# Kernel optimization log

Measured on AMD Instinct MI355X. Metric: run time of the kernel, lower is better.

The kernel has to match this reference:

```python
import jax, jax.numpy as jnp
import numpy as np

ANCHOR_NUM = 8
CLASS_NUM = 2
IN_DIM = 1024

def setup_inputs() -> dict:
    key = jax.random.key(0)
    k1, k2, k3, k4 = jax.random.split(key, 4)
    batch_input = jax.random.normal(k1, (64, 512, IN_DIM), dtype=jnp.float32)
    # labels in {-1, 0, 1}: -1 = padding, 0 = negative anchor, 1 = positive anchor
    anchor_labels = jax.random.randint(k2, (64, 512, ANCHOR_NUM), 0, 3, dtype=jnp.int64 if jax.config.read('jax_enable_x64') else jnp.int32) - 1
    lim = 1.0 / np.sqrt(IN_DIM)
    W = jax.random.uniform(k3, (IN_DIM, ANCHOR_NUM * CLASS_NUM), dtype=jnp.float32, minval=-lim, maxval=lim)
    b = jax.random.uniform(k4, (ANCHOR_NUM * CLASS_NUM,), dtype=jnp.float32, minval=-lim, maxval=lim)
    return {"batch_input": batch_input, "W": W, "b": b, "anchor_labels": anchor_labels}

def reference(batch_input, W, b, anchor_labels):
    B, S, _ = batch_input.shape
    # logits: (B, S, anchor_num, class_num)
    logits = (jnp.einsum('bsd,dk->bsk', batch_input, W) + b).reshape(B, S, ANCHOR_NUM, CLASS_NUM)
    predict_label = jnp.argmax(logits, axis=3)  # (B, S, A)
    valid = (anchor_labels != -1)
    labels = jnp.maximum(anchor_labels, 0)  # safe class index for padded entries
    logp = jax.nn.log_softmax(logits, axis=-1)
    nll = -jnp.take_along_axis(logp, labels[..., None].astype(jnp.int32), axis=-1)[..., 0]
    # CrossEntropyLoss (mean) over all non-padding anchors == eval-path gather + CE
    vf = valid.astype(logits.dtype)
    loss = jnp.sum(nll * vf) / jnp.maximum(jnp.sum(vf), 1.0)
    # candidate mask stands in for candidate_idx (positive predictions, non-padding)
    candidate_mask = (predict_label == 1) & valid
    return loss, predict_label, candidate_mask
```

## Files before the change

kernel.cpp:

```cpp
#include <hip/hip_runtime.h>
#include <math.h>


#define ROWS   64
#define NW     8
#define KSLICE 128
#define CHUNK  32
#define NCH    (KSLICE/CHUNK)
#define XSTR   36
#define RSTR   136

__global__ __launch_bounds__(512, 4)
void rpn_main(const float* __restrict__ x, const float* __restrict__ W,
              const float* __restrict__ b, const int* __restrict__ lab,
              float* __restrict__ out, float* __restrict__ ws)
{
    __shared__ float xs[NW * ROWS * XSTR];
    float* red = xs;

    const int tid  = threadIdx.x;
    const int lane = tid & 63;
    const int ks   = __builtin_amdgcn_readfirstlane(tid >> 6);
    const int row0 = blockIdx.x * ROWS;

    float* slab = xs + ks * (ROWS * XSTR);
    const float* gbase = x + (size_t)row0 * 1024 + ks * KSLICE;

    float acc[16];
#pragma unroll
    for (int c = 0; c < 16; ++c) acc[c] = 0.f;

    float4 pf[8];
#pragma unroll
    for (int j = 0; j < 8; ++j) {
        int fl = j * 64 + lane;
        pf[j] = *(const float4*)(gbase + (size_t)(fl >> 3) * 1024 + (fl & 7) * 4);
    }

#pragma unroll 1
    for (int ch = 0; ch < NCH; ++ch) {
#pragma unroll
        for (int j = 0; j < 8; ++j) {
            int fl = j * 64 + lane;
            *(float4*)(slab + (fl >> 3) * XSTR + (fl & 7) * 4) = pf[j];
        }
        if (ch + 1 < NCH) {
            const float* g = gbase + (ch + 1) * CHUNK;
#pragma unroll
            for (int j = 0; j < 8; ++j) {
                int fl = j * 64 + lane;
                pf[j] = *(const float4*)(g + (size_t)(fl >> 3) * 1024 + (fl & 7) * 4);
            }
        }
        const float* xrow = slab + lane * XSTR;
        const float* wk   = W + (size_t)(ks * KSLICE + ch * CHUNK) * 16;
#pragma unroll
        for (int t4 = 0; t4 < 8; ++t4) {
            float4 xq = *(const float4*)(xrow + t4 * 4);
#pragma unroll
            for (int i = 0; i < 4; ++i) {
                float xv = (&xq.x)[i];
                const float* wr = wk + (t4 * 4 + i) * 16;
#pragma unroll
                for (int c = 0; c < 16; ++c)
                    acc[c] = fmaf(xv, wr[c], acc[c]);
            }
        }
    }

    __syncthreads();
    {
        float* rp = red + lane * RSTR + ks * 16;
        *(float4*)(rp + 0)  = make_float4(acc[0],  acc[1],  acc[2],  acc[3]);
        *(float4*)(rp + 4)  = make_float4(acc[4],  acc[5],  acc[6],  acc[7]);
        *(float4*)(rp + 8)  = make_float4(acc[8],  acc[9],  acc[10], acc[11]);
        *(float4*)(rp + 12) = make_float4(acc[12], acc[13], acc[14], acc[15]);
    }
    __syncthreads();

    if (tid < ROWS) {
        const int row = row0 + tid;
        float L[16];
#pragma unroll
        for (int c = 0; c < 16; ++c) {
            float s = 0.f;
#pragma unroll
            for (int k = 0; k < NW; ++k) s += red[tid * RSTR + k * 16 + c];
            L[c] = s + b[c];
        }

        const int* labp  = lab + (size_t)row * 8;
        float*     predp = out + 1 + (size_t)row * 8;
        float*     maskp = out + 1 + 262144 + (size_t)row * 8;

        float lsum = 0.f, lcnt = 0.f;
#pragma unroll
        for (int a = 0; a < 8; ++a) {
            float l0 = L[2 * a], l1 = L[2 * a + 1];
            int   lb = labp[a];
            int   pred  = (l1 > l0) ? 1 : 0;
            int   valid = (lb != -1);
            float m   = fmaxf(l0, l1);
            float lse = m + logf(expf(l0 - m) + expf(l1 - m));
            float nll = lse - ((lb == 1) ? l1 : l0);
            if (valid) { lsum += nll; lcnt += 1.f; }
            predp[a] = (float)pred;
            maskp[a] = (pred && valid) ? 1.f : 0.f;
        }

#pragma unroll
        for (int off = 32; off > 0; off >>= 1) {
            lsum += __shfl_down(lsum, off, 64);
            lcnt += __shfl_down(lcnt, off, 64);
        }
        if (tid == 0) {
            atomicAdd(&ws[0], lsum);
            atomicAdd(&ws[1], lcnt);
        }
    }
}

__global__ void rpn_final(const float* __restrict__ ws, float* __restrict__ out)
{
    out[0] = ws[0] / fmaxf(ws[1], 1.f);
}

extern "C" void kernel_launch(void* const* d_in, const int* in_sizes, int n_in,
                              void* d_out, int out_size, void* d_ws, size_t ws_size,
                              hipStream_t stream)
{
    const float* x   = (const float*)d_in[0];
    const float* W   = (const float*)d_in[1];
    const float* b   = (const float*)d_in[2];
    const int*   lab = (const int*)d_in[3];
    float* out = (float*)d_out;
    float* ws  = (float*)d_ws;

    hipMemsetAsync(ws, 0, 2 * sizeof(float), stream);
    rpn_main<<<dim3(512), dim3(512), 0, stream>>>(x, W, b, lab, out, ws);
    rpn_final<<<dim3(1), dim3(1), 0, stream>>>(ws, out);
}
```

Measured before the change: 237.9 us.

## Keep W slice in registers, stream rows directly, fuse final loss division

Drops the LDS-staged x tile. Each lane now holds a 4x16 slice of W in registers and streams one row at a time straight from global memory with a two-deep prefetch. Per-row results are reduced across lanes with a butterfly shuffle, and the logits pass uses one thread per anchor. The separate finalize kernel is replaced by a last-block-done atomic counter. In exchange there is heavy shuffle work per row and less row parallelism per block (32 rows, 4 waves).

```diff
diff --git a/kernel.cpp b/kernel.cpp
--- a/kernel.cpp
+++ b/kernel.cpp
@@ -2,127 +2,162 @@
 #include <math.h>
 
 
-#define ROWS   64
-#define NW     8
-#define KSLICE 128
-#define CHUNK  32
-#define NCH    (KSLICE/CHUNK)
-#define XSTR   36
-#define RSTR   136
+#define RPB 32
 
-__global__ __launch_bounds__(512, 4)
+__global__ __launch_bounds__(256, 2)
 void rpn_main(const float* __restrict__ x, const float* __restrict__ W,
               const float* __restrict__ b, const int* __restrict__ lab,
               float* __restrict__ out, float* __restrict__ ws)
 {
-    __shared__ float xs[NW * ROWS * XSTR];
-    float* red = xs;
+    __shared__ float red[4 * RPB * 16];
+    __shared__ float rsum[8];
 
     const int tid  = threadIdx.x;
     const int lane = tid & 63;
-    const int ks   = __builtin_amdgcn_readfirstlane(tid >> 6);
-    const int row0 = blockIdx.x * ROWS;
+    const int s    = __builtin_amdgcn_readfirstlane(tid >> 6);
+    const int row0 = blockIdx.x * RPB;
 
-    float* slab = xs + ks * (ROWS * XSTR);
-    const float* gbase = x + (size_t)row0 * 1024 + ks * KSLICE;
-
-    float acc[16];
+    float4 wc0[4], wc1[4], wc2[4], wc3[4];
+    {
+        const float* wp = W + (size_t)(s * 256 + lane * 4) * 16;
 #pragma unroll
-    for (int c = 0; c < 16; ++c) acc[c] = 0.f;
-
-    float4 pf[8];
-#pragma unroll
-    for (int j = 0; j < 8; ++j) {
-        int fl = j * 64 + lane;
-        pf[j] = *(const float4*)(gbase + (size_t)(fl >> 3) * 1024 + (fl & 7) * 4);
-    }
-
-#pragma unroll 1
-    for (int ch = 0; ch < NCH; ++ch) {
-#pragma unroll
-        for (int j = 0; j < 8; ++j) {
-            int fl = j * 64 + lane;
-            *(float4*)(slab + (fl >> 3) * XSTR + (fl & 7) * 4) = pf[j];
-        }
-        if (ch + 1 < NCH) {
-            const float* g = gbase + (ch + 1) * CHUNK;
-#pragma unroll
-            for (int j = 0; j < 8; ++j) {
-                int fl = j * 64 + lane;
-                pf[j] = *(const float4*)(g + (size_t)(fl >> 3) * 1024 + (fl & 7) * 4);
-            }
-        }
-        const float* xrow = slab + lane * XSTR;
-        const float* wk   = W + (size_t)(ks * KSLICE + ch * CHUNK) * 16;
-#pragma unroll
-        for (int t4 = 0; t4 < 8; ++t4) {
-            float4 xq = *(const float4*)(xrow + t4 * 4);
-#pragma unroll
-            for (int i = 0; i < 4; ++i) {
-                float xv = (&xq.x)[i];
-                const float* wr = wk + (t4 * 4 + i) * 16;
-#pragma unroll
-                for (int c = 0; c < 16; ++c)
-                    acc[c] = fmaf(xv, wr[c], acc[c]);
-            }
+        for (int q = 0; q < 4; ++q) {
+            wc0[q] = *(const float4*)(wp +  0 + q * 4);
+            wc1[q] = *(const float4*)(wp + 16 + q * 4);
+            wc2[q] = *(const float4*)(wp + 32 + q * 4);
+            wc3[q] = *(const float4*)(wp + 48 + q * 4);
         }
     }
 
-    __syncthreads();
-    {
-        float* rp = red + lane * RSTR + ks * 16;
-        *(float4*)(rp + 0)  = make_float4(acc[0],  acc[1],  acc[2],  acc[3]);
-        *(float4*)(rp + 4)  = make_float4(acc[4],  acc[5],  acc[6],  acc[7]);
-        *(float4*)(rp + 8)  = make_float4(acc[8],  acc[9],  acc[10], acc[11]);
-        *(float4*)(rp + 12) = make_float4(acc[12], acc[13], acc[14], acc[15]);
+    const float* xp = x + (size_t)row0 * 1024 + s * 256 + lane * 4;
+
+    float4 pfA = *(const float4*)(xp);
+    float4 pfB = *(const float4*)(xp + 1024);
+
+#pragma unroll 2
+    for (int r = 0; r < RPB; ++r) {
+        float4 xv = pfA;
+        pfA = pfB;
+        if (r + 2 < RPB) pfB = *(const float4*)(xp + (size_t)(r + 2) * 1024);
+
+        const float xs0 = xv.x, xs1 = xv.y, xs2 = xv.z, xs3 = xv.w;
+        float acc[16];
+#pragma unroll
+        for (int q = 0; q < 4; ++q) {
+            acc[4*q+0] = xs0 * wc0[q].x;
+            acc[4*q+1] = xs0 * wc0[q].y;
+            acc[4*q+2] = xs0 * wc0[q].z;
+            acc[4*q+3] = xs0 * wc0[q].w;
+        }
+#pragma unroll
+        for (int q = 0; q < 4; ++q) {
+            acc[4*q+0] = fmaf(xs1, wc1[q].x, acc[4*q+0]);
+            acc[4*q+1] = fmaf(xs1, wc1[q].y, acc[4*q+1]);
+            acc[4*q+2] = fmaf(xs1, wc1[q].z, acc[4*q+2]);
+            acc[4*q+3] = fmaf(xs1, wc1[q].w, acc[4*q+3]);
+        }
+#pragma unroll
+        for (int q = 0; q < 4; ++q) {
+            acc[4*q+0] = fmaf(xs2, wc2[q].x, acc[4*q+0]);
+            acc[4*q+1] = fmaf(xs2, wc2[q].y, acc[4*q+1]);
+            acc[4*q+2] = fmaf(xs2, wc2[q].z, acc[4*q+2]);
+            acc[4*q+3] = fmaf(xs2, wc2[q].w, acc[4*q+3]);
+        }
+#pragma unroll
+        for (int q = 0; q < 4; ++q) {
+            acc[4*q+0] = fmaf(xs3, wc3[q].x, acc[4*q+0]);
+            acc[4*q+1] = fmaf(xs3, wc3[q].y, acc[4*q+1]);
+            acc[4*q+2] = fmaf(xs3, wc3[q].z, acc[4*q+2]);
+            acc[4*q+3] = fmaf(xs3, wc3[q].w, acc[4*q+3]);
+        }
+
+        const bool h5 = (lane & 32) != 0;
+        float k8[8];
+#pragma unroll
+        for (int c = 0; c < 8; ++c) {
+            float keep = h5 ? acc[c + 8] : acc[c];
+            float send = h5 ? acc[c]     : acc[c + 8];
+            k8[c] = keep + __shfl_xor(send, 32, 64);
+        }
+        const bool h4 = (lane & 16) != 0;
+        float k4[4];
+#pragma unroll
+        for (int c = 0; c < 4; ++c) {
+            float keep = h4 ? k8[c + 4] : k8[c];
+            float send = h4 ? k8[c]     : k8[c + 4];
+            k4[c] = keep + __shfl_xor(send, 16, 64);
+        }
+        const bool h3 = (lane & 8) != 0;
+        float k2[2];
+#pragma unroll
+        for (int c = 0; c < 2; ++c) {
+            float keep = h3 ? k4[c + 2] : k4[c];
+            float send = h3 ? k4[c]     : k4[c + 2];
+            k2[c] = keep + __shfl_xor(send, 8, 64);
+        }
+        const bool h2 = (lane & 4) != 0;
+        float keep1 = h2 ? k2[1] : k2[0];
+        float send1 = h2 ? k2[0] : k2[1];
+        float k1 = keep1 + __shfl_xor(send1, 4, 64);
+        k1 += __shfl_xor(k1, 2, 64);
+        k1 += __shfl_xor(k1, 1, 64);
+
+        if ((lane & 3) == 0)
+            red[(s * RPB + r) * 16 + (lane >> 2)] = k1;
     }
+
     __syncthreads();
 
-    if (tid < ROWS) {
-        const int row = row0 + tid;
-        float L[16];
-#pragma unroll
-        for (int c = 0; c < 16; ++c) {
-            float s = 0.f;
-#pragma unroll
-            for (int k = 0; k < NW; ++k) s += red[tid * RSTR + k * 16 + c];
-            L[c] = s + b[c];
-        }
+    {
+        const int row = tid >> 3;
+        const int a   = tid & 7;
+        const int gr  = row0 + row;
 
-        const int* labp  = lab + (size_t)row * 8;
-        float*     predp = out + 1 + (size_t)row * 8;
-        float*     maskp = out + 1 + 262144 + (size_t)row * 8;
+        const int i0 = row * 16 + 2 * a;
+        float l0 = red[0 * RPB * 16 + i0]     + red[1 * RPB * 16 + i0]
+                 + red[2 * RPB * 16 + i0]     + red[3 * RPB * 16 + i0]
+                 + b[2 * a];
+        float l1 = red[0 * RPB * 16 + i0 + 1] + red[1 * RPB * 16 + i0 + 1]
+                 + red[2 * RPB * 16 + i0 + 1] + red[3 * RPB * 16 + i0 + 1]
+                 + b[2 * a + 1];
 
-        float lsum = 0.f, lcnt = 0.f;
-#pragma unroll
-        for (int a = 0; a < 8; ++a) {
-            float l0 = L[2 * a], l1 = L[2 * a + 1];
-            int   lb = labp[a];
-            int   pred  = (l1 > l0) ? 1 : 0;
-            int   valid = (lb != -1);
-            float m   = fmaxf(l0, l1);
-            float lse = m + logf(expf(l0 - m) + expf(l1 - m));
-            float nll = lse - ((lb == 1) ? l1 : l0);
-            if (valid) { lsum += nll; lcnt += 1.f; }
-            predp[a] = (float)pred;
-            maskp[a] = (pred && valid) ? 1.f : 0.f;
-        }
+        const int lb    = lab[(size_t)gr * 8 + a];
+        const int pred  = (l1 > l0) ? 1 : 0;
+        const int valid = (lb != -1);
+        const float m   = fmaxf(l0, l1);
+        const float lse = m + logf(expf(l0 - m) + expf(l1 - m));
+        const float nll = lse - ((lb == 1) ? l1 : l0);
+        float lsum = valid ? nll : 0.f;
+        float lcnt = valid ? 1.f : 0.f;
+
+        out[1 + (size_t)row0 * 8 + tid]          = (float)pred;
+        out[1 + 262144 + (size_t)row0 * 8 + tid] = (pred && valid) ? 1.f : 0.f;
 
 #pragma unroll
         for (int off = 32; off > 0; off >>= 1) {
             lsum += __shfl_down(lsum, off, 64);
             lcnt += __shfl_down(lcnt, off, 64);
         }
-        if (tid == 0) {
-            atomicAdd(&ws[0], lsum);
-            atomicAdd(&ws[1], lcnt);
+        if (lane == 0) {
+            rsum[s * 2]     = lsum;
+            rsum[s * 2 + 1] = lcnt;
         }
     }
-}
+    __syncthreads();
 
-__global__ void rpn_final(const float* __restrict__ ws, float* __restrict__ out)
-{
-    out[0] = ws[0] / fmaxf(ws[1], 1.f);
+    if (tid == 0) {
+        float S = rsum[0] + rsum[2] + rsum[4] + rsum[6];
+        float C = rsum[1] + rsum[3] + rsum[5] + rsum[7];
+        atomicAdd(&ws[0], S);
+        atomicAdd(&ws[1], C);
+        __threadfence();
+        unsigned int old = atomicAdd((unsigned int*)(ws + 2), 1u);
+        if (old == gridDim.x - 1) {
+            float Sf = atomicAdd(&ws[0], 0.f);
+            float Cf = atomicAdd(&ws[1], 0.f);
+            out[0] = Sf / fmaxf(Cf, 1.f);
+        }
+    }
 }
 
 extern "C" void kernel_launch(void* const* d_in, const int* in_sizes, int n_in,
@@ -136,7 +171,6 @@
     float* out = (float*)d_out;
     float* ws  = (float*)d_ws;
 
-    hipMemsetAsync(ws, 0, 2 * sizeof(float), stream);
-    rpn_main<<<dim3(512), dim3(512), 0, stream>>>(x, W, b, lab, out, ws);
-    rpn_final<<<dim3(1), dim3(1), 0, stream>>>(ws, out);
+    hipMemsetAsync(ws, 0, 16, stream);
+    rpn_main<<<dim3(1024), dim3(256), 0, stream>>>(x, W, b, lab, out, ws);
 }
```

Measured after the change: 249.4 us. +4.9%, slower.
